# Kernel tuning notes

Measured on AMD Instinct MI355X. Metric: run time of the kernel, lower is better.

## Reference

```python
import jax, jax.numpy as jnp
import numpy as np

U, I, D, E, L = 100000, 50000, 64, 600000, 3
N = U + I  # total nodes in bipartite graph


def setup_inputs() -> dict:
    key = jax.random.key(0)
    k1, k2, k3, k4 = jax.random.split(key, 4)
    user_emb = jax.random.normal(k1, (U, D), dtype=jnp.float32) * 0.1
    item_emb = jax.random.normal(k2, (I, D), dtype=jnp.float32) * 0.1
    # random user-item interactions; symmetrize to build the (U+I)x(U+I) adjacency
    u = jax.random.randint(k3, (E,), 0, U)
    i = jax.random.randint(k4, (E,), 0, I) + U
    edge_src = jnp.concatenate([u, i])  # [2E]
    edge_dst = jnp.concatenate([i, u])  # [2E]
    # symmetric normalization: A_hat[s,d] = 1/sqrt(deg_s * deg_d)
    deg = jax.ops.segment_sum(jnp.ones((2 * E,), jnp.float32), edge_dst, num_segments=N)
    dinv = jnp.where(deg > 0, 1.0 / jnp.sqrt(deg), 0.0)
    edge_vals = dinv[edge_src] * dinv[edge_dst]
    return {
        "user_emb": user_emb,
        "item_emb": item_emb,
        "edge_src": edge_src,
        "edge_dst": edge_dst,
        "edge_vals": edge_vals,
    }


def reference(user_emb, item_emb, edge_src, edge_dst, edge_vals):
    # LightGCN propagation: ego_{k+1} = A_hat @ ego_k, then mean over the L layer outputs
    ego = jnp.concatenate([user_emb, item_emb], axis=0)  # [N, D]
    acc = jnp.zeros_like(ego)
    for _ in range(L):  # fixed small layer count
        msgs = edge_vals[:, None] * ego[edge_src]  # [2E, D] gather + scale
        ego = jax.ops.segment_sum(msgs, edge_dst, num_segments=N)  # SpMM via scatter-add
        acc = acc + ego
    mean_emb = acc / L
    return mean_emb[:U], mean_emb[U:]
```

## Files before the change

kernel.cpp:

```cpp
#include <hip/hip_runtime.h>

#define U_CNT 100000
#define I_CNT 50000
#define D_DIM 64
#define N_NODES 150000
#define CHUNK 2048
#define NBKT 586
#define SCAN_BLK 512
#define CCAP 3584

__device__ __forceinline__ float blo(unsigned u) { return __uint_as_float(u << 16); }
__device__ __forceinline__ float bhi(unsigned u) { return __uint_as_float(u & 0xFFFF0000u); }
__device__ __forceinline__ unsigned f2b(float f) {
    unsigned b = __float_as_uint(f);
    return (b + 0x7FFFu + ((b >> 16) & 1u)) >> 16;
}
__device__ __forceinline__ unsigned pack2(float a, float b) {
    return f2b(a) | (f2b(b) << 16);
}

__global__ void bucket_hist(const int* __restrict__ dst, int* __restrict__ H,
                            int NB_B, int nE,
                            const float4* __restrict__ user4,
                            const float4* __restrict__ item4,
                            uint2* __restrict__ ego0, int n4u, int n4) {
    __shared__ int h[NBKT];
    for (int i = threadIdx.x; i < NBKT; i += blockDim.x) h[i] = 0;
    __syncthreads();
    int b = blockIdx.x;
    int beg = b * CHUNK, end = min(nE, beg + CHUNK);
    for (int e = beg + (int)threadIdx.x; e < end; e += blockDim.x)
        atomicAdd(&h[dst[e] >> 8], 1);
    __syncthreads();
    for (int i = threadIdx.x; i < NBKT; i += blockDim.x) H[i * NB_B + b] = h[i];
    int gsz = gridDim.x * blockDim.x;
    for (int i = blockIdx.x * blockDim.x + threadIdx.x; i < n4; i += gsz) {
        float4 f = (i < n4u) ? user4[i] : item4[i - n4u];
        ego0[i] = make_uint2(pack2(f.x, f.y), pack2(f.z, f.w));
    }
}

__global__ void block_sums(const int* __restrict__ in, int* __restrict__ blksum, int n) {
    __shared__ int sm[SCAN_BLK];
    int i = blockIdx.x * SCAN_BLK + threadIdx.x;
    sm[threadIdx.x] = (i < n) ? in[i] : 0;
    __syncthreads();
    for (int off = SCAN_BLK / 2; off > 0; off >>= 1) {
        if (threadIdx.x < off) sm[threadIdx.x] += sm[threadIdx.x + off];
        __syncthreads();
    }
    if (threadIdx.x == 0) blksum[blockIdx.x] = sm[0];
}

__global__ void scan_blksums(const int* __restrict__ blksum, int* __restrict__ blkoff, int nb) {
    __shared__ int sm[1024];
    int t = threadIdx.x;
    int v = (t < nb) ? blksum[t] : 0;
    sm[t] = v;
    __syncthreads();
    for (int off = 1; off < 1024; off <<= 1) {
        int x = (t >= off) ? sm[t - off] : 0;
        __syncthreads();
        sm[t] += x;
        __syncthreads();
    }
    if (t < nb) blkoff[t] = sm[t] - v;
}

__global__ void scan_within(int* __restrict__ H, const int* __restrict__ blkoff, int n) {
    __shared__ int sm[SCAN_BLK];
    int i = blockIdx.x * SCAN_BLK + threadIdx.x;
    int t = threadIdx.x;
    int d = (i < n) ? H[i] : 0;
    sm[t] = d;
    __syncthreads();
    for (int off = 1; off < SCAN_BLK; off <<= 1) {
        int x = (t >= off) ? sm[t - off] : 0;
        __syncthreads();
        sm[t] += x;
        __syncthreads();
    }
    if (i < n) H[i] = blkoff[blockIdx.x] + sm[t] - d;
}

__global__ void bucket_scatter(const int* __restrict__ src, const int* __restrict__ dst,
                               const float* __restrict__ val, const int* __restrict__ Hs,
                               uint2* __restrict__ tmp, int NB_B, int nE) {
    __shared__ int cur[NBKT];
    int b = blockIdx.x;
    for (int i = threadIdx.x; i < NBKT; i += blockDim.x) cur[i] = Hs[i * NB_B + b];
    __syncthreads();
    int beg = b * CHUNK, end = min(nE, beg + CHUNK);
    for (int e = beg + (int)threadIdx.x; e < end; e += blockDim.x) {
        int d = dst[e];
        int pos = atomicAdd(&cur[d >> 8], 1);
        tmp[pos] = make_uint2((unsigned)src[e] | ((unsigned)(d & 255) << 18),
                              __float_as_uint(val[e]));
    }
}

__global__ void bucket_build(const int* __restrict__ Hs, const uint2* __restrict__ tmp,
                             int2* __restrict__ csr, int* __restrict__ row_ptr,
                             int NB_B, int nE) {
    __shared__ int hist[256];
    __shared__ int scanbuf[256];
    __shared__ int cur[256];
    __shared__ uint2 cache[CCAP];
    int bkt  = blockIdx.x;
    int base = Hs[(size_t)bkt * NB_B];
    int endp = (bkt + 1 < NBKT) ? Hs[(size_t)(bkt + 1) * NB_B] : nE;
    int size = endp - base;
    int nbins = min(256, N_NODES - bkt * 256);
    int t = threadIdx.x;

    hist[t] = 0;
    __syncthreads();
    bool cached = (size <= CCAP);
    for (int k = t; k < size; k += blockDim.x) {
        uint2 r = tmp[base + k];
        if (cached) cache[k] = r;
        atomicAdd(&hist[(r.x >> 18) & 255], 1);
    }
    __syncthreads();
    int v = hist[t];
    scanbuf[t] = v;
    __syncthreads();
    for (int off = 1; off < 256; off <<= 1) {
        int x = (t >= off) ? scanbuf[t - off] : 0;
        __syncthreads();
        scanbuf[t] += x;
        __syncthreads();
    }
    int ex = scanbuf[t] - v;
    if (t < nbins) row_ptr[bkt * 256 + t] = base + ex;
    cur[t] = ex;
    __syncthreads();
    if (bkt == NBKT - 1) {
        if (t == 0) row_ptr[N_NODES] = nE;
        if (t < 4)  csr[nE + t] = make_int2(0, 0);
    }
    for (int k = t; k < size; k += blockDim.x) {
        uint2 r = cached ? cache[k] : tmp[base + k];
        int f = (r.x >> 18) & 255;
        int p = atomicAdd(&cur[f], 1);
        csr[base + p] = make_int2((int)(r.x & 0x3FFFFu), (int)r.y);
    }
}

__device__ __forceinline__ void fma8(float (&acc)[8], float v, uint4 g) {
    acc[0] = fmaf(v, blo(g.x), acc[0]); acc[1] = fmaf(v, bhi(g.x), acc[1]);
    acc[2] = fmaf(v, blo(g.y), acc[2]); acc[3] = fmaf(v, bhi(g.y), acc[3]);
    acc[4] = fmaf(v, blo(g.z), acc[4]); acc[5] = fmaf(v, bhi(g.z), acc[5]);
    acc[6] = fmaf(v, blo(g.w), acc[6]); acc[7] = fmaf(v, bhi(g.w), acc[7]);
}

template <int FINAL>
__global__ void lgcn_spmm(const int* __restrict__ row_ptr,
                          const int2* __restrict__ csr,
                          const uint4* __restrict__ ego_in,
                          uint4* __restrict__ ego_out,
                          const uint4* __restrict__ egoA,
                          const uint4* __restrict__ egoB,
                          float4* __restrict__ out) {
    int node = (blockIdx.x * blockDim.x + threadIdx.x) >> 3;
    int l    = threadIdx.x & 7;
    if (node >= N_NODES) return;
    int beg = row_ptr[node];
    int end = row_ptr[node + 1];

    float a0[8] = {0, 0, 0, 0, 0, 0, 0, 0};
    float a1[8] = {0, 0, 0, 0, 0, 0, 0, 0};

    int2 e0 = csr[beg], e1 = csr[beg + 1], e2 = csr[beg + 2], e3 = csr[beg + 3];
    int j = beg;
    while (j + 4 <= end) {
        uint4 x0 = ego_in[(size_t)e0.x * 8 + l];
        uint4 x1 = ego_in[(size_t)e1.x * 8 + l];
        uint4 x2 = ego_in[(size_t)e2.x * 8 + l];
        uint4 x3 = ego_in[(size_t)e3.x * 8 + l];
        int2 n0 = csr[j + 4], n1 = csr[j + 5], n2 = csr[j + 6], n3 = csr[j + 7];
        fma8(a0, __int_as_float(e0.y), x0);
        fma8(a1, __int_as_float(e1.y), x1);
        fma8(a0, __int_as_float(e2.y), x2);
        fma8(a1, __int_as_float(e3.y), x3);
        e0 = n0; e1 = n1; e2 = n2; e3 = n3;
        j += 4;
    }
    int rem = end - j;
    if (rem > 0) fma8(a0, __int_as_float(e0.y), ego_in[(size_t)e0.x * 8 + l]);
    if (rem > 1) fma8(a1, __int_as_float(e1.y), ego_in[(size_t)e1.x * 8 + l]);
    if (rem > 2) fma8(a0, __int_as_float(e2.y), ego_in[(size_t)e2.x * 8 + l]);

    float acc[8];
#pragma unroll
    for (int k = 0; k < 8; ++k) acc[k] = a0[k] + a1[k];

    if (!FINAL) {
        uint4 r;
        r.x = pack2(acc[0], acc[1]); r.y = pack2(acc[2], acc[3]);
        r.z = pack2(acc[4], acc[5]); r.w = pack2(acc[6], acc[7]);
        ego_out[(size_t)node * 8 + l] = r;
    } else {
        uint4 a = egoA[(size_t)node * 8 + l];
        uint4 b = egoB[(size_t)node * 8 + l];
        const float s = 1.0f / 3.0f;
        float4 o0, o1;
        o0.x = (blo(a.x) + blo(b.x) + acc[0]) * s;
        o0.y = (bhi(a.x) + bhi(b.x) + acc[1]) * s;
        o0.z = (blo(a.y) + blo(b.y) + acc[2]) * s;
        o0.w = (bhi(a.y) + bhi(b.y) + acc[3]) * s;
        o1.x = (blo(a.z) + blo(b.z) + acc[4]) * s;
        o1.y = (bhi(a.z) + bhi(b.z) + acc[5]) * s;
        o1.z = (blo(a.w) + blo(b.w) + acc[6]) * s;
        o1.w = (bhi(a.w) + bhi(b.w) + acc[7]) * s;
        size_t ob = (size_t)node * 16 + 2 * l;
        out[ob]     = o0;
        out[ob + 1] = o1;
    }
}

static inline size_t align_up(size_t x, size_t a) { return (x + a - 1) & ~(a - 1); }

extern "C" void kernel_launch(void* const* d_in, const int* in_sizes, int n_in,
                              void* d_out, int out_size, void* d_ws, size_t ws_size,
                              hipStream_t stream) {
    const float* user_emb  = (const float*)d_in[0];
    const float* item_emb  = (const float*)d_in[1];
    const int*   edge_src  = (const int*)d_in[2];
    const int*   edge_dst  = (const int*)d_in[3];
    const float* edge_vals = (const float*)d_in[4];
    const int    nE        = in_sizes[2];

    float* out = (float*)d_out;
    const size_t nd = (size_t)N_NODES * D_DIM;

    const int NB_B = (nE + CHUNK - 1) / CHUNK;
    const int nH   = NBKT * NB_B;
    const int NBs  = (nH + SCAN_BLK - 1) / SCAN_BLK;

    size_t off = 0;
    char* base = (char*)d_ws;
    int2*  csr     = (int2*)(base + off);  off = align_up(off + (size_t)(nE + 4) * sizeof(int2), 256);
    int*   row_ptr = (int*)(base + off);   off = align_up(off + (size_t)(N_NODES + 1) * 4, 256);
    uint2* tmp     = (uint2*)(base + off); off = align_up(off + (size_t)nE * sizeof(uint2), 256);
    int*   H       = (int*)(base + off);   off = align_up(off + (size_t)nH * 4, 256);
    int*   blksum  = (int*)(base + off);   off = align_up(off + (size_t)NBs * 4, 256);
    int*   blkoff  = (int*)(base + off);   off = align_up(off + (size_t)NBs * 4, 256);
    uint4* ego0    = (uint4*)(base + off); off = align_up(off + (size_t)N_NODES * 128, 256);
    uint4* ego_a   = (uint4*)(base + off); off = align_up(off + (size_t)N_NODES * 128, 256);
    uint4* ego_b   = (uint4*)(base + off); off = align_up(off + (size_t)N_NODES * 128, 256);

    const int block = 256;
    const int n4  = (int)(nd / 4);
    const int n4u = U_CNT * D_DIM / 4;

    bucket_hist<<<NB_B, block, 0, stream>>>(edge_dst, H, NB_B, nE,
        (const float4*)user_emb, (const float4*)item_emb, (uint2*)ego0, n4u, n4);
    block_sums<<<NBs, SCAN_BLK, 0, stream>>>(H, blksum, nH);
    scan_blksums<<<1, 1024, 0, stream>>>(blksum, blkoff, NBs);
    scan_within<<<NBs, SCAN_BLK, 0, stream>>>(H, blkoff, nH);
    bucket_scatter<<<NB_B, block, 0, stream>>>(edge_src, edge_dst, edge_vals, H, tmp, NB_B, nE);
    bucket_build<<<NBKT, block, 0, stream>>>(H, tmp, csr, row_ptr, NB_B, nE);

    const size_t threads = (size_t)N_NODES * 8;
    const int spmm_grid = (int)((threads + block - 1) / block);

    lgcn_spmm<0><<<spmm_grid, block, 0, stream>>>(
        row_ptr, csr, ego0, ego_a, nullptr, nullptr, nullptr);
    lgcn_spmm<0><<<spmm_grid, block, 0, stream>>>(
        row_ptr, csr, ego_a, ego_b, nullptr, nullptr, nullptr);
    lgcn_spmm<1><<<spmm_grid, block, 0, stream>>>(
        row_ptr, csr, ego_b, nullptr, ego_a, ego_b, (float4*)out);
}
```

Measured before the change: 235.9 us.

## Fuse three SpMM layers into one persistent kernel with grid barriers

Replaces the three separate per-layer SpMM launches with a single persistent kernel of 512 blocks. The blocks grid-stride over nodes and synchronise between layers with an atomic-counter grid barrier. This removes two kernel launch gaps and the tail drain between layers. In exchange it uses a fixed, smaller grid that may hide less latency on irregular gathers, and it relies on all 512 blocks being co-resident, or the barrier deadlocks. It also adds a memset.

```diff
diff --git a/kernel.cpp b/kernel.cpp
--- a/kernel.cpp
+++ b/kernel.cpp
@@ -8,6 +8,7 @@
 #define NBKT 586
 #define SCAN_BLK 512
 #define CCAP 3584
+#define FUSE_GRID 512
 
 __device__ __forceinline__ float blo(unsigned u) { return __uint_as_float(u << 16); }
 __device__ __forceinline__ float bhi(unsigned u) { return __uint_as_float(u & 0xFFFF0000u); }
@@ -154,69 +155,95 @@
     acc[6] = fmaf(v, blo(g.w), acc[6]); acc[7] = fmaf(v, bhi(g.w), acc[7]);
 }
 
+__device__ __forceinline__ void grid_bar(int* bar, int target) {
+    __syncthreads();
+    if (threadIdx.x == 0) {
+        __hip_atomic_fetch_add(bar, 1, __ATOMIC_ACQ_REL, __HIP_MEMORY_SCOPE_AGENT);
+        while (__hip_atomic_load(bar, __ATOMIC_ACQUIRE, __HIP_MEMORY_SCOPE_AGENT) < target)
+            __builtin_amdgcn_s_sleep(4);
+    }
+    __syncthreads();
+}
+
 template <int FINAL>
-__global__ void lgcn_spmm(const int* __restrict__ row_ptr,
-                          const int2* __restrict__ csr,
-                          const uint4* __restrict__ ego_in,
-                          uint4* __restrict__ ego_out,
-                          const uint4* __restrict__ egoA,
-                          const uint4* __restrict__ egoB,
-                          float4* __restrict__ out) {
-    int node = (blockIdx.x * blockDim.x + threadIdx.x) >> 3;
-    int l    = threadIdx.x & 7;
-    if (node >= N_NODES) return;
-    int beg = row_ptr[node];
-    int end = row_ptr[node + 1];
-
-    float a0[8] = {0, 0, 0, 0, 0, 0, 0, 0};
-    float a1[8] = {0, 0, 0, 0, 0, 0, 0, 0};
-
-    int2 e0 = csr[beg], e1 = csr[beg + 1], e2 = csr[beg + 2], e3 = csr[beg + 3];
-    int j = beg;
-    while (j + 4 <= end) {
-        uint4 x0 = ego_in[(size_t)e0.x * 8 + l];
-        uint4 x1 = ego_in[(size_t)e1.x * 8 + l];
-        uint4 x2 = ego_in[(size_t)e2.x * 8 + l];
-        uint4 x3 = ego_in[(size_t)e3.x * 8 + l];
-        int2 n0 = csr[j + 4], n1 = csr[j + 5], n2 = csr[j + 6], n3 = csr[j + 7];
-        fma8(a0, __int_as_float(e0.y), x0);
-        fma8(a1, __int_as_float(e1.y), x1);
-        fma8(a0, __int_as_float(e2.y), x2);
-        fma8(a1, __int_as_float(e3.y), x3);
-        e0 = n0; e1 = n1; e2 = n2; e3 = n3;
-        j += 4;
-    }
-    int rem = end - j;
-    if (rem > 0) fma8(a0, __int_as_float(e0.y), ego_in[(size_t)e0.x * 8 + l]);
-    if (rem > 1) fma8(a1, __int_as_float(e1.y), ego_in[(size_t)e1.x * 8 + l]);
-    if (rem > 2) fma8(a0, __int_as_float(e2.y), ego_in[(size_t)e2.x * 8 + l]);
-
-    float acc[8];
+__device__ __forceinline__ void spmm_rows(int g0, int ngroups, int l,
+                                          const int* __restrict__ row_ptr,
+                                          const int2* __restrict__ csr,
+                                          const uint4* __restrict__ ego_in,
+                                          uint4* __restrict__ ego_out,
+                                          const uint4* __restrict__ egoA,
+                                          const uint4* __restrict__ egoB,
+                                          float4* __restrict__ out) {
+    for (int node = g0; node < N_NODES; node += ngroups) {
+        int beg = row_ptr[node];
+        int end = row_ptr[node + 1];
+        float a0[8] = {0, 0, 0, 0, 0, 0, 0, 0};
+        float a1[8] = {0, 0, 0, 0, 0, 0, 0, 0};
+        int2 e0 = csr[beg], e1 = csr[beg + 1], e2 = csr[beg + 2], e3 = csr[beg + 3];
+        int j = beg;
+        while (j + 4 <= end) {
+            uint4 x0 = ego_in[(size_t)e0.x * 8 + l];
+            uint4 x1 = ego_in[(size_t)e1.x * 8 + l];
+            uint4 x2 = ego_in[(size_t)e2.x * 8 + l];
+            uint4 x3 = ego_in[(size_t)e3.x * 8 + l];
+            int2 n0 = csr[j + 4], n1 = csr[j + 5], n2 = csr[j + 6], n3 = csr[j + 7];
+            fma8(a0, __int_as_float(e0.y), x0);
+            fma8(a1, __int_as_float(e1.y), x1);
+            fma8(a0, __int_as_float(e2.y), x2);
+            fma8(a1, __int_as_float(e3.y), x3);
+            e0 = n0; e1 = n1; e2 = n2; e3 = n3;
+            j += 4;
+        }
+        int rem = end - j;
+        if (rem > 0) fma8(a0, __int_as_float(e0.y), ego_in[(size_t)e0.x * 8 + l]);
+        if (rem > 1) fma8(a1, __int_as_float(e1.y), ego_in[(size_t)e1.x * 8 + l]);
+        if (rem > 2) fma8(a0, __int_as_float(e2.y), ego_in[(size_t)e2.x * 8 + l]);
+
+        float acc[8];
 #pragma unroll
-    for (int k = 0; k < 8; ++k) acc[k] = a0[k] + a1[k];
-
-    if (!FINAL) {
-        uint4 r;
-        r.x = pack2(acc[0], acc[1]); r.y = pack2(acc[2], acc[3]);
-        r.z = pack2(acc[4], acc[5]); r.w = pack2(acc[6], acc[7]);
-        ego_out[(size_t)node * 8 + l] = r;
-    } else {
-        uint4 a = egoA[(size_t)node * 8 + l];
-        uint4 b = egoB[(size_t)node * 8 + l];
-        const float s = 1.0f / 3.0f;
-        float4 o0, o1;
-        o0.x = (blo(a.x) + blo(b.x) + acc[0]) * s;
-        o0.y = (bhi(a.x) + bhi(b.x) + acc[1]) * s;
-        o0.z = (blo(a.y) + blo(b.y) + acc[2]) * s;
-        o0.w = (bhi(a.y) + bhi(b.y) + acc[3]) * s;
-        o1.x = (blo(a.z) + blo(b.z) + acc[4]) * s;
-        o1.y = (bhi(a.z) + bhi(b.z) + acc[5]) * s;
-        o1.z = (blo(a.w) + blo(b.w) + acc[6]) * s;
-        o1.w = (bhi(a.w) + bhi(b.w) + acc[7]) * s;
-        size_t ob = (size_t)node * 16 + 2 * l;
-        out[ob]     = o0;
-        out[ob + 1] = o1;
-    }
+        for (int k = 0; k < 8; ++k) acc[k] = a0[k] + a1[k];
+
+        if (!FINAL) {
+            uint4 r;
+            r.x = pack2(acc[0], acc[1]); r.y = pack2(acc[2], acc[3]);
+            r.z = pack2(acc[4], acc[5]); r.w = pack2(acc[6], acc[7]);
+            ego_out[(size_t)node * 8 + l] = r;
+        } else {
+            uint4 a = egoA[(size_t)node * 8 + l];
+            uint4 b = egoB[(size_t)node * 8 + l];
+            const float s = 1.0f / 3.0f;
+            float4 o0, o1;
+            o0.x = (blo(a.x) + blo(b.x) + acc[0]) * s;
+            o0.y = (bhi(a.x) + bhi(b.x) + acc[1]) * s;
+            o0.z = (blo(a.y) + blo(b.y) + acc[2]) * s;
+            o0.w = (bhi(a.y) + bhi(b.y) + acc[3]) * s;
+            o1.x = (blo(a.z) + blo(b.z) + acc[4]) * s;
+            o1.y = (bhi(a.z) + bhi(b.z) + acc[5]) * s;
+            o1.z = (blo(a.w) + blo(b.w) + acc[6]) * s;
+            o1.w = (bhi(a.w) + bhi(b.w) + acc[7]) * s;
+            size_t ob = (size_t)node * 16 + 2 * l;
+            out[ob]     = o0;
+            out[ob + 1] = o1;
+        }
+    }
+}
+
+__global__ __launch_bounds__(256, 2)
+void lgcn_spmm_fused(const int* __restrict__ row_ptr,
+                     const int2* __restrict__ csr,
+                     const uint4* __restrict__ ego0,
+                     uint4* __restrict__ ego_a,
+                     uint4* __restrict__ ego_b,
+                     float4* __restrict__ out,
+                     int* __restrict__ bar) {
+    const int ngroups = (gridDim.x * blockDim.x) >> 3;
+    const int g0 = (blockIdx.x * blockDim.x + threadIdx.x) >> 3;
+    const int l  = threadIdx.x & 7;
+    spmm_rows<0>(g0, ngroups, l, row_ptr, csr, ego0, ego_a, nullptr, nullptr, nullptr);
+    grid_bar(bar, (int)gridDim.x);
+    spmm_rows<0>(g0, ngroups, l, row_ptr, csr, ego_a, ego_b, nullptr, nullptr, nullptr);
+    grid_bar(bar, 2 * (int)gridDim.x);
+    spmm_rows<1>(g0, ngroups, l, row_ptr, csr, ego_b, nullptr, ego_a, ego_b, out);
 }
 
 static inline size_t align_up(size_t x, size_t a) { return (x + a - 1) & ~(a - 1); }
@@ -249,10 +276,13 @@
     uint4* ego0    = (uint4*)(base + off); off = align_up(off + (size_t)N_NODES * 128, 256);
     uint4* ego_a   = (uint4*)(base + off); off = align_up(off + (size_t)N_NODES * 128, 256);
     uint4* ego_b   = (uint4*)(base + off); off = align_up(off + (size_t)N_NODES * 128, 256);
+    int*   bar     = (int*)(base + off);   off = align_up(off + 256, 256);
 
     const int block = 256;
     const int n4  = (int)(nd / 4);
     const int n4u = U_CNT * D_DIM / 4;
+
+    hipMemsetAsync(bar, 0, 64, stream);
 
     bucket_hist<<<NB_B, block, 0, stream>>>(edge_dst, H, NB_B, nE,
         (const float4*)user_emb, (const float4*)item_emb, (uint2*)ego0, n4u, n4);
@@ -262,13 +292,6 @@
     bucket_scatter<<<NB_B, block, 0, stream>>>(edge_src, edge_dst, edge_vals, H, tmp, NB_B, nE);
     bucket_build<<<NBKT, block, 0, stream>>>(H, tmp, csr, row_ptr, NB_B, nE);
 
-    const size_t threads = (size_t)N_NODES * 8;
-    const int spmm_grid = (int)((threads + block - 1) / block);
-
-    lgcn_spmm<0><<<spmm_grid, block, 0, stream>>>(
-        row_ptr, csr, ego0, ego_a, nullptr, nullptr, nullptr);
-    lgcn_spmm<0><<<spmm_grid, block, 0, stream>>>(
-        row_ptr, csr, ego_a, ego_b, nullptr, nullptr, nullptr);
-    lgcn_spmm<1><<<spmm_grid, block, 0, stream>>>(
-        row_ptr, csr, ego_b, nullptr, ego_a, ego_b, (float4*)out);
-}
+    lgcn_spmm_fused<<<FUSE_GRID, block, 0, stream>>>(
+        row_ptr, csr, ego0, ego_a, ego_b, (float4*)out, bar);
+}
```

New measurement: 411.4 us. 74.4% more time.
